# Optimization experiments

Measured on AMD Instinct MI355X. Metric: run time of the kernel, lower is better.

Reference implementation:

```python
import jax, jax.numpy as jnp
import numpy as np

C = 256
CK = C // 8  # query/key channels = 32


def setup_inputs() -> dict:
    key = jax.random.key(0)
    ks = jax.random.split(key, 7)
    sc = 0.05
    x = jax.random.normal(ks[0], (4, C, 64, 64), dtype=jnp.float32)
    Wq = jax.random.normal(ks[1], (CK, C), dtype=jnp.float32) * sc
    bq = jax.random.normal(ks[2], (CK,), dtype=jnp.float32) * sc
    Wk = jax.random.normal(ks[3], (CK, C), dtype=jnp.float32) * sc
    bk = jax.random.normal(ks[4], (CK,), dtype=jnp.float32) * sc
    Wv = jax.random.normal(ks[5], (C, C), dtype=jnp.float32) * sc
    bv = jax.random.normal(ks[6], (C,), dtype=jnp.float32) * sc
    gamma = jnp.array([0.5], dtype=jnp.float32)  # nonzero so output/grads are nontrivial
    return {"x": x, "Wq": Wq, "bq": bq, "Wk": Wk, "bk": bk, "Wv": Wv, "bv": bv, "gamma": gamma}


def reference(x, Wq, bq, Wk, bk, Wv, bv, gamma):
    B, Cc, H, W = x.shape
    xf = x.reshape(B, Cc, H * W)  # [B, C, N]
    # 1x1 conv1d == channel-wise matmul
    f = jnp.einsum('kc,bcn->bkn', Wq, xf) + bq[None, :, None]  # [B, CK, N]
    g = jnp.einsum('kc,bcn->bkn', Wk, xf) + bk[None, :, None]  # [B, CK, N]
    h = jnp.einsum('oc,bcn->bon', Wv, xf) + bv[None, :, None]  # [B, C, N]
    # unscaled attention scores: s[b,i,j] = sum_k f[b,k,i] g[b,k,j]
    s = jnp.einsum('bki,bkj->bij', f, g)  # [B, N, N]
    beta = jax.nn.softmax(s, axis=1)      # softmax over query-side axis i (dim=1)
    o = jnp.einsum('bci,bij->bcj', h, beta)  # [B, C, N]
    o = gamma[0] * o
    return o.reshape(B, Cc, H, W)
```

## Files before the change

### kernel.cpp

```cpp
#include <hip/hip_runtime.h>
#include <math.h>

#define BB 4
#define CC 256
#define CKK 32
#define NN 4096
#define TI 32
#define NT (NN / TI)
#define NP (NT / 2)
#define SM_OFF 40.0f

typedef __attribute__((ext_vector_type(8))) short short8v;
typedef __attribute__((ext_vector_type(4))) short short4v;
typedef __attribute__((ext_vector_type(4))) float f32x4;

static __device__ inline unsigned short f2bf(float x) {
    union { float f; unsigned u; } v; v.f = x;
    unsigned r = v.u + 0x7fffu + ((v.u >> 16) & 1u);
    return (unsigned short)(r >> 16);
}
static __device__ inline float bf2f(unsigned short h) {
    union { unsigned u; float f; } v; v.u = ((unsigned)h) << 16;
    return v.f;
}

__global__ __launch_bounds__(256) void prep_w(
    const float* __restrict__ Wq, const float* __restrict__ Wk,
    const float* __restrict__ Wv, unsigned short* __restrict__ Wbf)
{
    int o = blockIdx.x * 256 + threadIdx.x;
    int rb   = o >> 12;
    int rem  = o & 4095;
    int k    = rem >> 9;
    int lane = (rem >> 3) & 63;
    int e    = rem & 7;
    int row  = rb * 16 + (lane & 15);
    int c    = k * 32 + (lane >> 4) * 8 + e;
    float v;
    if (row < 32)      v = Wq[row * 256 + c];
    else if (row < 64) v = Wk[(row - 32) * 256 + c];
    else               v = Wv[(row - 64) * 256 + c];
    Wbf[o] = f2bf(v);
}

__global__ __launch_bounds__(256, 4) void proj_kernel(
    const float* __restrict__ x,
    const unsigned short* __restrict__ Wbf,
    const float* __restrict__ bq, const float* __restrict__ bk,
    const float* __restrict__ bv,
    unsigned short* __restrict__ fF, unsigned short* __restrict__ gT,
    unsigned short* __restrict__ hF)
{
    __shared__ unsigned short xsh[32 * 264];
    __shared__ unsigned short xsl[32 * 264];

    const int t = threadIdx.x;
    const int b = blockIdx.x >> 7;
    const int n_b = (blockIdx.x & 127) * 32;
    const int lane = t & 63;
    const int wave = t >> 6;
    const int jl = lane & 15;
    const int quad = lane >> 4;

    {
        const int q = t & 7, cb = t >> 3;
        #pragma unroll
        for (int cc = 0; cc < 8; ++cc) {
            int c = cb + cc * 32;
            float4 v = *(const float4*)(x + ((size_t)b * CC + c) * NN + n_b + q * 4);
            float vv[4] = {v.x, v.y, v.z, v.w};
            #pragma unroll
            for (int e = 0; e < 4; ++e) {
                int n = q * 4 + e;
                unsigned short h = f2bf(vv[e]);
                unsigned short l = f2bf(vv[e] - bf2f(h));
                xsh[n * 264 + c] = h;
                xsl[n * 264 + c] = l;
            }
        }
    }
    __syncthreads();

    const int rowbase_w = wave * 80;
    #pragma unroll 1
    for (int nt = 0; nt < 2; ++nt) {
        short8v bhi[8], blo[8];
        #pragma unroll
        for (int k = 0; k < 8; ++k) {
            bhi[k] = *(const short8v*)&xsh[(nt * 16 + jl) * 264 + k * 32 + quad * 8];
            blo[k] = *(const short8v*)&xsl[(nt * 16 + jl) * 264 + k * 32 + quad * 8];
        }
        const int ng = n_b + nt * 16 + jl;
        const int it  = ng >> 5;
        const int il  = ng & 31;
        const int ihh = (ng >> 4) & 1;
        #pragma unroll 1
        for (int mt = 0; mt < 5; ++mt) {
            int rowbase = rowbase_w + mt * 16;
            const int rb = rowbase >> 4;
            const unsigned short* wf = Wbf + (size_t)rb * 8 * 512;
            f32x4 acch = (f32x4){0.f, 0.f, 0.f, 0.f};
            f32x4 accl = (f32x4){0.f, 0.f, 0.f, 0.f};
            #pragma unroll
            for (int k = 0; k < 8; ++k) {
                short8v a = *(const short8v*)(wf + (size_t)k * 512 + lane * 8);
                acch = __builtin_amdgcn_mfma_f32_16x16x32_bf16(a, bhi[k], acch, 0, 0, 0);
                accl = __builtin_amdgcn_mfma_f32_16x16x32_bf16(a, blo[k], accl, 0, 0, 0);
            }
            f32x4 acc;
            #pragma unroll
            for (int r = 0; r < 4; ++r) acc[r] = acch[r] + accl[r];
            int rlo = rowbase + quad * 4;
            if (rowbase < 32) {
                float4 bias = *(const float4*)(bq + rlo);
                short4v o;
                o[0] = (short)f2bf(acc[0] + bias.x); o[1] = (short)f2bf(acc[1] + bias.y);
                o[2] = (short)f2bf(acc[2] + bias.z); o[3] = (short)f2bf(acc[3] + bias.w);
                size_t dst = (((size_t)b * NT + it) * 2 + ihh) * 512
                           + (size_t)((rlo >> 3) * 16 + (ng & 15)) * 8 + (rlo & 7);
                *(short4v*)(fF + dst) = o;
            } else if (rowbase < 64) {
                float4 bias = *(const float4*)(bk + rlo - 32);
                short4v o;
                o[0] = (short)f2bf(acc[0] + bias.x); o[1] = (short)f2bf(acc[1] + bias.y);
                o[2] = (short)f2bf(acc[2] + bias.z); o[3] = (short)f2bf(acc[3] + bias.w);
                *(short4v*)(gT + ((size_t)b * NN + ng) * CKK + (rlo - 32)) = o;
            } else {
                const float* bp = bv + rlo - 64;
                #pragma unroll
                for (int r = 0; r < 4; ++r) {
                    int c = rlo - 64 + r;
                    size_t dst = (((size_t)b * NT + it) * 16 + (c >> 4)) * 512
                               + (size_t)((il >> 3) * 16 + (c & 15)) * 8 + (il & 7);
                    hF[dst] = f2bf(acc[r] + bp[r]);
                }
            }
        }
    }
}

__global__ __launch_bounds__(1024, 4) void attn_kernel(
    const unsigned short* __restrict__ fF,
    const unsigned short* __restrict__ gT,
    const unsigned short* __restrict__ hF,
    const float* __restrict__ gamma,
    float* __restrict__ out)
{
    __shared__ unsigned short pa[2][2][4][512];
    __shared__ float ls[8][2][16];
    __shared__ float ls2[4][16];

    const int t = threadIdx.x;
    const int lane = t & 63;
    const int wave = t >> 6;
    const int bi = blockIdx.x;
    const int b  = bi & 3;
    const int j0 = (bi >> 2) * 64;
    const int jl = lane & 15;
    const int quad = lane >> 4;

    const unsigned short* fFb = fF + (size_t)b * NT * 2 * 512;
    const unsigned short* hFb = hF + (size_t)b * NT * 16 * 512;

    const f32x4 zoff = (f32x4){-SM_OFF, -SM_OFF, -SM_OFF, -SM_OFF};

    if (wave < 8) {
        const int sub = wave >> 2;
        const int ihp = (wave >> 1) & 1;
        const int jcp = wave & 1;
        const int Lw = ((ihp * 2 + (quad >> 1)) * 16 + jl) * 8 + (quad & 1) * 4;

        short8v bg0 = *(const short8v*)(gT + ((size_t)b * NN + j0 + (2 * jcp) * 16 + jl) * CKK + quad * 8);
        short8v bg1 = *(const short8v*)(gT + ((size_t)b * NN + j0 + (2 * jcp + 1) * 16 + jl) * CKK + quad * 8);

        float l0 = 0.f, l1 = 0.f;

        short8v af = *(const short8v*)(fFb + ((size_t)sub * 2 + ihp) * 512 + lane * 8);
        short8v afn = *(const short8v*)(fFb + ((size_t)(2 + sub) * 2 + ihp) * 512 + lane * 8);
        {
            f32x4 s0 = __builtin_amdgcn_mfma_f32_16x16x32_bf16(af, bg0, zoff, 0, 0, 0);
            f32x4 s1 = __builtin_amdgcn_mfma_f32_16x16x32_bf16(af, bg1, zoff, 0, 0, 0);
            float e0 = __expf(s0[0]), e1 = __expf(s0[1]), e2 = __expf(s0[2]), e3 = __expf(s0[3]);
            float f0 = __expf(s1[0]), f1 = __expf(s1[1]), f2 = __expf(s1[2]), f3 = __expf(s1[3]);
            l0 += (e0 + e1) + (e2 + e3);
            l1 += (f0 + f1) + (f2 + f3);
            unsigned p01, p23, q01, q23;
            asm("v_cvt_pk_bf16_f32 %0, %1, %2" : "=v"(p01) : "v"(e0), "v"(e1));
            asm("v_cvt_pk_bf16_f32 %0, %1, %2" : "=v"(p23) : "v"(e2), "v"(e3));
            asm("v_cvt_pk_bf16_f32 %0, %1, %2" : "=v"(q01) : "v"(f0), "v"(f1));
            asm("v_cvt_pk_bf16_f32 %0, %1, %2" : "=v"(q23) : "v"(f2), "v"(f3));
            uint2 pw; pw.x = p01; pw.y = p23;
            uint2 qw; qw.x = q01; qw.y = q23;
            *(uint2*)&pa[0][sub][2 * jcp][Lw] = pw;
            *(uint2*)&pa[0][sub][2 * jcp + 1][Lw] = qw;
        }
        asm volatile("s_waitcnt lgkmcnt(0)" ::: "memory");
        __builtin_amdgcn_s_barrier();
        asm volatile("" ::: "memory");

        #pragma unroll 1
        for (int p = 0; p < NP; ++p) {
            const int buf = p & 1;
            if (p + 1 < NP) {
                f32x4 s0 = __builtin_amdgcn_mfma_f32_16x16x32_bf16(afn, bg0, zoff, 0, 0, 0);
                f32x4 s1 = __builtin_amdgcn_mfma_f32_16x16x32_bf16(afn, bg1, zoff, 0, 0, 0);
                {
                    const int p2 = (p + 2 < NP ? p + 2 : NP - 1);
                    afn = *(const short8v*)(fFb + ((size_t)(2 * p2 + sub) * 2 + ihp) * 512 + lane * 8);
                }
                float e0 = __expf(s0[0]), e1 = __expf(s0[1]), e2 = __expf(s0[2]), e3 = __expf(s0[3]);
                float f0 = __expf(s1[0]), f1 = __expf(s1[1]), f2 = __expf(s1[2]), f3 = __expf(s1[3]);
                l0 += (e0 + e1) + (e2 + e3);
                l1 += (f0 + f1) + (f2 + f3);
                unsigned p01, p23, q01, q23;
                asm("v_cvt_pk_bf16_f32 %0, %1, %2" : "=v"(p01) : "v"(e0), "v"(e1));
                asm("v_cvt_pk_bf16_f32 %0, %1, %2" : "=v"(p23) : "v"(e2), "v"(e3));
                asm("v_cvt_pk_bf16_f32 %0, %1, %2" : "=v"(q01) : "v"(f0), "v"(f1));
                asm("v_cvt_pk_bf16_f32 %0, %1, %2" : "=v"(q23) : "v"(f2), "v"(f3));
                uint2 pw; pw.x = p01; pw.y = p23;
                uint2 qw; qw.x = q01; qw.y = q23;
                *(uint2*)&pa[buf ^ 1][sub][2 * jcp][Lw] = pw;
                *(uint2*)&pa[buf ^ 1][sub][2 * jcp + 1][Lw] = qw;
            }
            asm volatile("s_waitcnt lgkmcnt(0)" ::: "memory");
            __builtin_amdgcn_s_barrier();
            asm volatile("" ::: "memory");
        }

        l0 += __shfl_xor(l0, 16, 64);
        l0 += __shfl_xor(l0, 32, 64);
        l1 += __shfl_xor(l1, 16, 64);
        l1 += __shfl_xor(l1, 32, 64);
        if (quad == 0) { ls[wave][0][jl] = l0; ls[wave][1][jl] = l1; }
        __syncthreads();
        if (wave < 4 && quad == 0) {
            const int jc = wave;
            const int jp = jc >> 1, sl = jc & 1;
            ls2[jc][jl] = gamma[0] / (((ls[jp][sl][jl] + ls[jp + 2][sl][jl])
                                     + (ls[jp + 4][sl][jl] + ls[jp + 6][sl][jl])));
        }
        __syncthreads();
    } else {
        const int cw = wave - 8;
        const int cg0 = cw * 2;

        f32x4 acc[8];
        #pragma unroll
        for (int q = 0; q < 8; ++q) acc[q] = (f32x4){0.f, 0.f, 0.f, 0.f};

        short8v ahA0 = *(const short8v*)(hFb + ((size_t)0 * 16 + cg0 + 0) * 512 + lane * 8);
        short8v ahA1 = *(const short8v*)(hFb + ((size_t)0 * 16 + cg0 + 1) * 512 + lane * 8);
        short8v ahB0 = *(const short8v*)(hFb + ((size_t)1 * 16 + cg0 + 0) * 512 + lane * 8);
        short8v ahB1 = *(const short8v*)(hFb + ((size_t)1 * 16 + cg0 + 1) * 512 + lane * 8);
        short8v anA0 = *(const short8v*)(hFb + ((size_t)2 * 16 + cg0 + 0) * 512 + lane * 8);
        short8v anA1 = *(const short8v*)(hFb + ((size_t)2 * 16 + cg0 + 1) * 512 + lane * 8);
        short8v anB0 = *(const short8v*)(hFb + ((size_t)3 * 16 + cg0 + 0) * 512 + lane * 8);
        short8v anB1 = *(const short8v*)(hFb + ((size_t)3 * 16 + cg0 + 1) * 512 + lane * 8);
        asm volatile("s_waitcnt lgkmcnt(0)" ::: "memory");
        __builtin_amdgcn_s_barrier();
        asm volatile("" ::: "memory");

        #pragma unroll 1
        for (int p = 0; p < NP; ++p) {
            const int buf = p & 1;

            const int pq = (p + 2 < NP ? p + 2 : NP - 1);
            short8v aqA0 = *(const short8v*)(hFb + ((size_t)(2 * pq) * 16 + cg0 + 0) * 512 + lane * 8);
            short8v aqA1 = *(const short8v*)(hFb + ((size_t)(2 * pq) * 16 + cg0 + 1) * 512 + lane * 8);
            short8v aqB0 = *(const short8v*)(hFb + ((size_t)(2 * pq + 1) * 16 + cg0 + 0) * 512 + lane * 8);
            short8v aqB1 = *(const short8v*)(hFb + ((size_t)(2 * pq + 1) * 16 + cg0 + 1) * 512 + lane * 8);

            __builtin_amdgcn_s_setprio(1);
            #pragma unroll
            for (int jc2 = 0; jc2 < 4; ++jc2) {
                short8v bpA = *(const short8v*)&pa[buf][0][jc2][lane * 8];
                acc[jc2 * 2 + 0] = __builtin_amdgcn_mfma_f32_16x16x32_bf16(ahA0, bpA, acc[jc2 * 2 + 0], 0, 0, 0);
                acc[jc2 * 2 + 1] = __builtin_amdgcn_mfma_f32_16x16x32_bf16(ahA1, bpA, acc[jc2 * 2 + 1], 0, 0, 0);
                short8v bpB = *(const short8v*)&pa[buf][1][jc2][lane * 8];
                acc[jc2 * 2 + 0] = __builtin_amdgcn_mfma_f32_16x16x32_bf16(ahB0, bpB, acc[jc2 * 2 + 0], 0, 0, 0);
                acc[jc2 * 2 + 1] = __builtin_amdgcn_mfma_f32_16x16x32_bf16(ahB1, bpB, acc[jc2 * 2 + 1], 0, 0, 0);
            }
            __builtin_amdgcn_s_setprio(0);

            asm volatile("s_waitcnt lgkmcnt(0)" ::: "memory");
            __builtin_amdgcn_s_barrier();
            asm volatile("" ::: "memory");

            ahA0 = anA0; ahA1 = anA1; ahB0 = anB0; ahB1 = anB1;
            anA0 = aqA0; anA1 = aqA1; anB0 = aqB0; anB1 = aqB1;
        }

        __syncthreads();
        __syncthreads();

        #pragma unroll
        for (int jc2 = 0; jc2 < 4; ++jc2) {
            float sc = ls2[jc2][jl];
            #pragma unroll
            for (int cc = 0; cc < 2; ++cc) {
                f32x4 a = acc[jc2 * 2 + cc];
                size_t addr = ((size_t)b * CC + cw * 32 + cc * 16 + quad * 4) * NN + j0 + jc2 * 16 + jl;
                #pragma unroll
                for (int r = 0; r < 4; ++r)
                    out[addr + (size_t)r * NN] = a[r] * sc;
            }
        }
    }
}

extern "C" void kernel_launch(void* const* d_in, const int* in_sizes, int n_in,
                              void* d_out, int out_size, void* d_ws, size_t ws_size,
                              hipStream_t stream) {
    const float* x     = (const float*)d_in[0];
    const float* Wq    = (const float*)d_in[1];
    const float* bq    = (const float*)d_in[2];
    const float* Wk    = (const float*)d_in[3];
    const float* bk    = (const float*)d_in[4];
    const float* Wv    = (const float*)d_in[5];
    const float* bv    = (const float*)d_in[6];
    const float* gamma = (const float*)d_in[7];
    float* out = (float*)d_out;

    unsigned short* Wbf = (unsigned short*)d_ws;
    unsigned short* fF  = Wbf + 320 * 256;
    unsigned short* gT  = fF + (size_t)BB * NN * CKK;
    unsigned short* hF  = gT + (size_t)BB * NN * CKK;

    prep_w<<<320, 256, 0, stream>>>(Wq, Wk, Wv, Wbf);
    proj_kernel<<<BB * (NN / 32), 256, 0, stream>>>(x, Wbf, bq, bk, bv, fF, gT, hF);
    attn_kernel<<<BB * (NN / 64), 1024, 0, stream>>>(fF, gT, hF, gamma, out);
}
```

Measured before the change: 139.9 us.

## Process four key tiles per barrier stage and coalesce h-projection stores

The attention kernel now has each softmax-producer wave handle all four j-columns for one i-tile, so every pipeline stage covers 128 query rows instead of 64. This halves the number of block-wide barriers, and the consumer loop ping-pongs two register sets of h fragments with explicit prefetch. The projection kernel stages h outputs through shared memory so each lane writes one contiguous short4 instead of scattered 2-byte stores. The cost is a larger shared-memory footprint for the P buffers and more live VGPRs for the h fragments, which may hurt occupancy under the 1024-thread launch bound.

```diff
diff --git a/kernel.cpp b/kernel.cpp
--- a/kernel.cpp
+++ b/kernel.cpp
@@ -7,7 +7,9 @@
 #define NN 4096
 #define TI 32
 #define NT (NN / TI)
-#define NP (NT / 2)
+#define NQ (NT / 4)
+#define FQS (4 * 2 * 512)
+#define HQS (4 * 16 * 512)
 #define SM_OFF 40.0f
 
 typedef __attribute__((ext_vector_type(8))) short short8v;
@@ -53,6 +55,7 @@
 {
     __shared__ unsigned short xsh[32 * 264];
     __shared__ unsigned short xsl[32 * 264];
+    __shared__ unsigned short hstg[4][256];
 
     const int t = threadIdx.x;
     const int b = blockIdx.x >> 7;
@@ -61,6 +64,7 @@
     const int wave = t >> 6;
     const int jl = lane & 15;
     const int quad = lane >> 4;
+    const int itb = n_b >> 5;
 
     {
         const int q = t & 7, cb = t >> 3;
@@ -91,8 +95,6 @@
             blo[k] = *(const short8v*)&xsl[(nt * 16 + jl) * 264 + k * 32 + quad * 8];
         }
         const int ng = n_b + nt * 16 + jl;
-        const int it  = ng >> 5;
-        const int il  = ng & 31;
         const int ihh = (ng >> 4) & 1;
         #pragma unroll 1
         for (int mt = 0; mt < 5; ++mt) {
@@ -116,7 +118,7 @@
                 short4v o;
                 o[0] = (short)f2bf(acc[0] + bias.x); o[1] = (short)f2bf(acc[1] + bias.y);
                 o[2] = (short)f2bf(acc[2] + bias.z); o[3] = (short)f2bf(acc[3] + bias.w);
-                size_t dst = (((size_t)b * NT + it) * 2 + ihh) * 512
+                size_t dst = (((size_t)b * NT + itb) * 2 + ihh) * 512
                            + (size_t)((rlo >> 3) * 16 + (ng & 15)) * 8 + (rlo & 7);
                 *(short4v*)(fF + dst) = o;
             } else if (rowbase < 64) {
@@ -127,13 +129,15 @@
                 *(short4v*)(gT + ((size_t)b * NN + ng) * CKK + (rlo - 32)) = o;
             } else {
                 const float* bp = bv + rlo - 64;
+                const int cgh = (rowbase - 64) >> 4;
                 #pragma unroll
                 for (int r = 0; r < 4; ++r) {
-                    int c = rlo - 64 + r;
-                    size_t dst = (((size_t)b * NT + it) * 16 + (c >> 4)) * 512
-                               + (size_t)((il >> 3) * 16 + (c & 15)) * 8 + (il & 7);
-                    hF[dst] = f2bf(acc[r] + bp[r]);
+                    int rel = ((jl >> 3) * 128) + (quad * 4 + r) * 8 + (jl & 7);
+                    hstg[wave][rel] = f2bf(acc[r] + bp[r]);
                 }
+                short4v v = *(const short4v*)&hstg[wave][lane * 4];
+                size_t hbase = (((size_t)b * NT + itb) * 16 + cgh) * 512 + nt * 256;
+                *(short4v*)(hF + hbase + lane * 4) = v;
             }
         }
     }
@@ -146,8 +150,8 @@
     const float* __restrict__ gamma,
     float* __restrict__ out)
 {
-    __shared__ unsigned short pa[2][2][4][512];
-    __shared__ float ls[8][2][16];
+    __shared__ unsigned short pa[2][4][4][512];
+    __shared__ float ls[8][4][16];
     __shared__ float ls2[4][16];
 
     const int t = threadIdx.x;
@@ -165,79 +169,87 @@
     const f32x4 zoff = (f32x4){-SM_OFF, -SM_OFF, -SM_OFF, -SM_OFF};
 
     if (wave < 8) {
-        const int sub = wave >> 2;
-        const int ihp = (wave >> 1) & 1;
-        const int jcp = wave & 1;
+        const int sub = wave >> 1;
+        const int ihp = wave & 1;
         const int Lw = ((ihp * 2 + (quad >> 1)) * 16 + jl) * 8 + (quad & 1) * 4;
 
-        short8v bg0 = *(const short8v*)(gT + ((size_t)b * NN + j0 + (2 * jcp) * 16 + jl) * CKK + quad * 8);
-        short8v bg1 = *(const short8v*)(gT + ((size_t)b * NN + j0 + (2 * jcp + 1) * 16 + jl) * CKK + quad * 8);
-
-        float l0 = 0.f, l1 = 0.f;
-
-        short8v af = *(const short8v*)(fFb + ((size_t)sub * 2 + ihp) * 512 + lane * 8);
-        short8v afn = *(const short8v*)(fFb + ((size_t)(2 + sub) * 2 + ihp) * 512 + lane * 8);
-        {
-            f32x4 s0 = __builtin_amdgcn_mfma_f32_16x16x32_bf16(af, bg0, zoff, 0, 0, 0);
-            f32x4 s1 = __builtin_amdgcn_mfma_f32_16x16x32_bf16(af, bg1, zoff, 0, 0, 0);
-            float e0 = __expf(s0[0]), e1 = __expf(s0[1]), e2 = __expf(s0[2]), e3 = __expf(s0[3]);
-            float f0 = __expf(s1[0]), f1 = __expf(s1[1]), f2 = __expf(s1[2]), f3 = __expf(s1[3]);
-            l0 += (e0 + e1) + (e2 + e3);
-            l1 += (f0 + f1) + (f2 + f3);
-            unsigned p01, p23, q01, q23;
-            asm("v_cvt_pk_bf16_f32 %0, %1, %2" : "=v"(p01) : "v"(e0), "v"(e1));
-            asm("v_cvt_pk_bf16_f32 %0, %1, %2" : "=v"(p23) : "v"(e2), "v"(e3));
-            asm("v_cvt_pk_bf16_f32 %0, %1, %2" : "=v"(q01) : "v"(f0), "v"(f1));
-            asm("v_cvt_pk_bf16_f32 %0, %1, %2" : "=v"(q23) : "v"(f2), "v"(f3));
-            uint2 pw; pw.x = p01; pw.y = p23;
-            uint2 qw; qw.x = q01; qw.y = q23;
-            *(uint2*)&pa[0][sub][2 * jcp][Lw] = pw;
-            *(uint2*)&pa[0][sub][2 * jcp + 1][Lw] = qw;
-        }
+        short8v bg0 = *(const short8v*)(gT + ((size_t)b * NN + j0 + 0 * 16 + jl) * CKK + quad * 8);
+        short8v bg1 = *(const short8v*)(gT + ((size_t)b * NN + j0 + 1 * 16 + jl) * CKK + quad * 8);
+        short8v bg2 = *(const short8v*)(gT + ((size_t)b * NN + j0 + 2 * 16 + jl) * CKK + quad * 8);
+        short8v bg3 = *(const short8v*)(gT + ((size_t)b * NN + j0 + 3 * 16 + jl) * CKK + quad * 8);
+
+        float l0 = 0.f, l1 = 0.f, l2 = 0.f, l3 = 0.f;
+
+        const unsigned short* fp = fFb + (size_t)(sub * 2 + ihp) * 512 + (size_t)lane * 8;
+
+        #define PRODUCE(AF, PB)                                                           \
+        {                                                                                 \
+            f32x4 s0 = __builtin_amdgcn_mfma_f32_16x16x32_bf16(AF, bg0, zoff, 0, 0, 0);   \
+            f32x4 s1 = __builtin_amdgcn_mfma_f32_16x16x32_bf16(AF, bg1, zoff, 0, 0, 0);   \
+            f32x4 s2 = __builtin_amdgcn_mfma_f32_16x16x32_bf16(AF, bg2, zoff, 0, 0, 0);   \
+            f32x4 s3 = __builtin_amdgcn_mfma_f32_16x16x32_bf16(AF, bg3, zoff, 0, 0, 0);   \
+            float e0, e1, e2, e3; unsigned p01, p23; uint2 pw;                            \
+            e0 = __expf(s0[0]); e1 = __expf(s0[1]); e2 = __expf(s0[2]); e3 = __expf(s0[3]);\
+            l0 += (e0 + e1) + (e2 + e3);                                                  \
+            asm("v_cvt_pk_bf16_f32 %0, %1, %2" : "=v"(p01) : "v"(e0), "v"(e1));           \
+            asm("v_cvt_pk_bf16_f32 %0, %1, %2" : "=v"(p23) : "v"(e2), "v"(e3));           \
+            pw.x = p01; pw.y = p23; *(uint2*)&pa[PB][sub][0][Lw] = pw;                    \
+            e0 = __expf(s1[0]); e1 = __expf(s1[1]); e2 = __expf(s1[2]); e3 = __expf(s1[3]);\
+            l1 += (e0 + e1) + (e2 + e3);                                                  \
+            asm("v_cvt_pk_bf16_f32 %0, %1, %2" : "=v"(p01) : "v"(e0), "v"(e1));           \
+            asm("v_cvt_pk_bf16_f32 %0, %1, %2" : "=v"(p23) : "v"(e2), "v"(e3));           \
+            pw.x = p01; pw.y = p23; *(uint2*)&pa[PB][sub][1][Lw] = pw;                    \
+            e0 = __expf(s2[0]); e1 = __expf(s2[1]); e2 = __expf(s2[2]); e3 = __expf(s2[3]);\
+            l2 += (e0 + e1) + (e2 + e3);                                                  \
+            asm("v_cvt_pk_bf16_f32 %0, %1, %2" : "=v"(p01) : "v"(e0), "v"(e1));           \
+            asm("v_cvt_pk_bf16_f32 %0, %1, %2" : "=v"(p23) : "v"(e2), "v"(e3));           \
+            pw.x = p01; pw.y = p23; *(uint2*)&pa[PB][sub][2][Lw] = pw;                    \
+            e0 = __expf(s3[0]); e1 = __expf(s3[1]); e2 = __expf(s3[2]); e3 = __expf(s3[3]);\
+            l3 += (e0 + e1) + (e2 + e3);                                                  \
+            asm("v_cvt_pk_bf16_f32 %0, %1, %2" : "=v"(p01) : "v"(e0), "v"(e1));           \
+            asm("v_cvt_pk_bf16_f32 %0, %1, %2" : "=v"(p23) : "v"(e2), "v"(e3));           \
+            pw.x = p01; pw.y = p23; *(uint2*)&pa[PB][sub][3][Lw] = pw;                    \
+        }
+
+        short8v afA = *(const short8v*)fp; fp += FQS;
+        short8v afB = *(const short8v*)fp; fp += FQS;
+        PRODUCE(afA, 0)
         asm volatile("s_waitcnt lgkmcnt(0)" ::: "memory");
         __builtin_amdgcn_s_barrier();
         asm volatile("" ::: "memory");
 
         #pragma unroll 1
-        for (int p = 0; p < NP; ++p) {
-            const int buf = p & 1;
-            if (p + 1 < NP) {
-                f32x4 s0 = __builtin_amdgcn_mfma_f32_16x16x32_bf16(afn, bg0, zoff, 0, 0, 0);
-                f32x4 s1 = __builtin_amdgcn_mfma_f32_16x16x32_bf16(afn, bg1, zoff, 0, 0, 0);
-                {
-                    const int p2 = (p + 2 < NP ? p + 2 : NP - 1);
-                    afn = *(const short8v*)(fFb + ((size_t)(2 * p2 + sub) * 2 + ihp) * 512 + lane * 8);
-                }
-                float e0 = __expf(s0[0]), e1 = __expf(s0[1]), e2 = __expf(s0[2]), e3 = __expf(s0[3]);
-                float f0 = __expf(s1[0]), f1 = __expf(s1[1]), f2 = __expf(s1[2]), f3 = __expf(s1[3]);
-                l0 += (e0 + e1) + (e2 + e3);
-                l1 += (f0 + f1) + (f2 + f3);
-                unsigned p01, p23, q01, q23;
-                asm("v_cvt_pk_bf16_f32 %0, %1, %2" : "=v"(p01) : "v"(e0), "v"(e1));
-                asm("v_cvt_pk_bf16_f32 %0, %1, %2" : "=v"(p23) : "v"(e2), "v"(e3));
-                asm("v_cvt_pk_bf16_f32 %0, %1, %2" : "=v"(q01) : "v"(f0), "v"(f1));
-                asm("v_cvt_pk_bf16_f32 %0, %1, %2" : "=v"(q23) : "v"(f2), "v"(f3));
-                uint2 pw; pw.x = p01; pw.y = p23;
-                uint2 qw; qw.x = q01; qw.y = q23;
-                *(uint2*)&pa[buf ^ 1][sub][2 * jcp][Lw] = pw;
-                *(uint2*)&pa[buf ^ 1][sub][2 * jcp + 1][Lw] = qw;
-            }
+        for (int q = 0; q < NQ; q += 2) {
+            PRODUCE(afB, 1)
+            if (q + 2 < NQ) { afA = *(const short8v*)fp; fp += FQS; }
             asm volatile("s_waitcnt lgkmcnt(0)" ::: "memory");
             __builtin_amdgcn_s_barrier();
             asm volatile("" ::: "memory");
-        }
-
-        l0 += __shfl_xor(l0, 16, 64);
-        l0 += __shfl_xor(l0, 32, 64);
-        l1 += __shfl_xor(l1, 16, 64);
-        l1 += __shfl_xor(l1, 32, 64);
-        if (quad == 0) { ls[wave][0][jl] = l0; ls[wave][1][jl] = l1; }
+
+            if (q + 2 < NQ) {
+                PRODUCE(afA, 0)
+                if (q + 3 < NQ) { afB = *(const short8v*)fp; fp += FQS; }
+            }
+            asm volatile("s_waitcnt lgkmcnt(0)" ::: "memory");
+            __builtin_amdgcn_s_barrier();
+            asm volatile("" ::: "memory");
+        }
+        #undef PRODUCE
+
+        l0 += __shfl_xor(l0, 16, 64); l0 += __shfl_xor(l0, 32, 64);
+        l1 += __shfl_xor(l1, 16, 64); l1 += __shfl_xor(l1, 32, 64);
+        l2 += __shfl_xor(l2, 16, 64); l2 += __shfl_xor(l2, 32, 64);
+        l3 += __shfl_xor(l3, 16, 64); l3 += __shfl_xor(l3, 32, 64);
+        if (quad == 0) {
+            ls[wave][0][jl] = l0; ls[wave][1][jl] = l1;
+            ls[wave][2][jl] = l2; ls[wave][3][jl] = l3;
+        }
         __syncthreads();
         if (wave < 4 && quad == 0) {
             const int jc = wave;
-            const int jp = jc >> 1, sl = jc & 1;
-            ls2[jc][jl] = gamma[0] / (((ls[jp][sl][jl] + ls[jp + 2][sl][jl])
-                                     + (ls[jp + 4][sl][jl] + ls[jp + 6][sl][jl])));
+            float s = ((ls[0][jc][jl] + ls[1][jc][jl]) + (ls[2][jc][jl] + ls[3][jc][jl]))
+                    + ((ls[4][jc][jl] + ls[5][jc][jl]) + (ls[6][jc][jl] + ls[7][jc][jl]));
+            ls2[jc][jl] = gamma[0] / s;
         }
         __syncthreads();
     } else {
@@ -248,47 +260,64 @@
         #pragma unroll
         for (int q = 0; q < 8; ++q) acc[q] = (f32x4){0.f, 0.f, 0.f, 0.f};
 
-        short8v ahA0 = *(const short8v*)(hFb + ((size_t)0 * 16 + cg0 + 0) * 512 + lane * 8);
-        short8v ahA1 = *(const short8v*)(hFb + ((size_t)0 * 16 + cg0 + 1) * 512 + lane * 8);
-        short8v ahB0 = *(const short8v*)(hFb + ((size_t)1 * 16 + cg0 + 0) * 512 + lane * 8);
-        short8v ahB1 = *(const short8v*)(hFb + ((size_t)1 * 16 + cg0 + 1) * 512 + lane * 8);
-        short8v anA0 = *(const short8v*)(hFb + ((size_t)2 * 16 + cg0 + 0) * 512 + lane * 8);
-        short8v anA1 = *(const short8v*)(hFb + ((size_t)2 * 16 + cg0 + 1) * 512 + lane * 8);
-        short8v anB0 = *(const short8v*)(hFb + ((size_t)3 * 16 + cg0 + 0) * 512 + lane * 8);
-        short8v anB1 = *(const short8v*)(hFb + ((size_t)3 * 16 + cg0 + 1) * 512 + lane * 8);
+        const unsigned short* hq = hFb + (size_t)cg0 * 512 + (size_t)lane * 8;
+
+        #define HLOAD(D0,D1,D2,D3,D4,D5,D6,D7, P)                      \
+            D0 = *(const short8v*)(P + 0 * 8192 + 0 * 512);            \
+            D1 = *(const short8v*)(P + 0 * 8192 + 1 * 512);            \
+            D2 = *(const short8v*)(P + 1 * 8192 + 0 * 512);            \
+            D3 = *(const short8v*)(P + 1 * 8192 + 1 * 512);            \
+            D4 = *(const short8v*)(P + 2 * 8192 + 0 * 512);            \
+            D5 = *(const short8v*)(P + 2 * 8192 + 1 * 512);            \
+            D6 = *(const short8v*)(P + 3 * 8192 + 0 * 512);            \
+            D7 = *(const short8v*)(P + 3 * 8192 + 1 * 512);
+
+        #define PV(H0,H1,H2,H3,H4,H5,H6,H7, PB)                                                     \
+        {                                                                                           \
+            __builtin_amdgcn_s_setprio(1);                                                          \
+            _Pragma("unroll")                                                                       \
+            for (int jc2 = 0; jc2 < 4; ++jc2) {                                                     \
+                short8v bp0 = *(const short8v*)&pa[PB][0][jc2][lane * 8];                           \
+                acc[jc2 * 2 + 0] = __builtin_amdgcn_mfma_f32_16x16x32_bf16(H0, bp0, acc[jc2 * 2 + 0], 0, 0, 0); \
+                acc[jc2 * 2 + 1] = __builtin_amdgcn_mfma_f32_16x16x32_bf16(H1, bp0, acc[jc2 * 2 + 1], 0, 0, 0); \
+                short8v bp1 = *(const short8v*)&pa[PB][1][jc2][lane * 8];                           \
+                acc[jc2 * 2 + 0] = __builtin_amdgcn_mfma_f32_16x16x32_bf16(H2, bp1, acc[jc2 * 2 + 0], 0, 0, 0); \
+                acc[jc2 * 2 + 1] = __builtin_amdgcn_mfma_f32_16x16x32_bf16(H3, bp1, acc[jc2 * 2 + 1], 0, 0, 0); \
+                short8v bp2 = *(const short8v*)&pa[PB][2][jc2][lane * 8];                           \
+                acc[jc2 * 2 + 0] = __builtin_amdgcn_mfma_f32_16x16x32_bf16(H4, bp2, acc[jc2 * 2 + 0], 0, 0, 0); \
+                acc[jc2 * 2 + 1] = __builtin_amdgcn_mfma_f32_16x16x32_bf16(H5, bp2, acc[jc2 * 2 + 1], 0, 0, 0); \
+                short8v bp3 = *(const short8v*)&pa[PB][3][jc2][lane * 8];                           \
+                acc[jc2 * 2 + 0] = __builtin_amdgcn_mfma_f32_16x16x32_bf16(H6, bp3, acc[jc2 * 2 + 0], 0, 0, 0); \
+                acc[jc2 * 2 + 1] = __builtin_amdgcn_mfma_f32_16x16x32_bf16(H7, bp3, acc[jc2 * 2 + 1], 0, 0, 0); \
+            }                                                                                       \
+            __builtin_amdgcn_s_setprio(0);                                                          \
+        }
+
+        short8v hA0, hA1, hA2, hA3, hA4, hA5, hA6, hA7;
+        short8v hB0, hB1, hB2, hB3, hB4, hB5, hB6, hB7;
+
+        HLOAD(hA0,hA1,hA2,hA3,hA4,hA5,hA6,hA7, hq)  hq += HQS;
+        HLOAD(hB0,hB1,hB2,hB3,hB4,hB5,hB6,hB7, hq)  hq += HQS;
         asm volatile("s_waitcnt lgkmcnt(0)" ::: "memory");
         __builtin_amdgcn_s_barrier();
         asm volatile("" ::: "memory");
 
         #pragma unroll 1
-        for (int p = 0; p < NP; ++p) {
-            const int buf = p & 1;
-
-            const int pq = (p + 2 < NP ? p + 2 : NP - 1);
-            short8v aqA0 = *(const short8v*)(hFb + ((size_t)(2 * pq) * 16 + cg0 + 0) * 512 + lane * 8);
-            short8v aqA1 = *(const short8v*)(hFb + ((size_t)(2 * pq) * 16 + cg0 + 1) * 512 + lane * 8);
-            short8v aqB0 = *(const short8v*)(hFb + ((size_t)(2 * pq + 1) * 16 + cg0 + 0) * 512 + lane * 8);
-            short8v aqB1 = *(const short8v*)(hFb + ((size_t)(2 * pq + 1) * 16 + cg0 + 1) * 512 + lane * 8);
-
-            __builtin_amdgcn_s_setprio(1);
-            #pragma unroll
-            for (int jc2 = 0; jc2 < 4; ++jc2) {
-                short8v bpA = *(const short8v*)&pa[buf][0][jc2][lane * 8];
-                acc[jc2 * 2 + 0] = __builtin_amdgcn_mfma_f32_16x16x32_bf16(ahA0, bpA, acc[jc2 * 2 + 0], 0, 0, 0);
-                acc[jc2 * 2 + 1] = __builtin_amdgcn_mfma_f32_16x16x32_bf16(ahA1, bpA, acc[jc2 * 2 + 1], 0, 0, 0);
-                short8v bpB = *(const short8v*)&pa[buf][1][jc2][lane * 8];
-                acc[jc2 * 2 + 0] = __builtin_amdgcn_mfma_f32_16x16x32_bf16(ahB0, bpB, acc[jc2 * 2 + 0], 0, 0, 0);
-                acc[jc2 * 2 + 1] = __builtin_amdgcn_mfma_f32_16x16x32_bf16(ahB1, bpB, acc[jc2 * 2 + 1], 0, 0, 0);
-            }
-            __builtin_amdgcn_s_setprio(0);
-
+        for (int q = 0; q < NQ; q += 2) {
+            PV(hA0,hA1,hA2,hA3,hA4,hA5,hA6,hA7, 0)
+            if (q + 2 < NQ) { HLOAD(hA0,hA1,hA2,hA3,hA4,hA5,hA6,hA7, hq)  hq += HQS; }
             asm volatile("s_waitcnt lgkmcnt(0)" ::: "memory");
             __builtin_amdgcn_s_barrier();
             asm volatile("" ::: "memory");
 
-            ahA0 = anA0; ahA1 = anA1; ahB0 = anB0; ahB1 = anB1;
-            anA0 = aqA0; anA1 = aqA1; anB0 = aqB0; anB1 = aqB1;
-        }
+            PV(hB0,hB1,hB2,hB3,hB4,hB5,hB6,hB7, 1)
+            if (q + 3 < NQ) { HLOAD(hB0,hB1,hB2,hB3,hB4,hB5,hB6,hB7, hq)  hq += HQS; }
+            asm volatile("s_waitcnt lgkmcnt(0)" ::: "memory");
+            __builtin_amdgcn_s_barrier();
+            asm volatile("" ::: "memory");
+        }
+        #undef HLOAD
+        #undef PV
 
         __syncthreads();
         __syncthreads();
```

After: 136.1 us (median of 2 runs). 2.7% less time.
